# Optimization experiments

Measured on AMD Instinct MI355X. Metric: run time of the kernel, lower is better.

## Reference

```python
import jax, jax.numpy as jnp
from jax import lax
import numpy as np

ROI = 7  # roi_size


def _extract_rois(feat, coords):
    """Faithful port of extract_roi_features: clamp a 7x7 window to image bounds,
    then bilinearly resize the (possibly smaller) crop back to 7x7
    (F.interpolate, mode='bilinear', align_corners=False)."""
    B, C, H, W = feat.shape
    half = ROI // 2

    def axis_idx(c, size):
        start = jnp.maximum(0, c - half)                  # [B,A]
        end = jnp.minimum(size, c + half + 1)
        Li = end - start                                  # crop length (int) [B,A]
        L = Li.astype(feat.dtype)[..., None]              # [B,A,1]
        j = jnp.arange(ROI, dtype=feat.dtype)
        # align_corners=False source coordinate, clamped into the crop
        src = jnp.clip((j + 0.5) * L / ROI - 0.5, 0.0, L - 1.0)  # [B,A,7]
        i0 = jnp.floor(src).astype(jnp.int32)
        i1 = jnp.minimum(i0 + 1, Li[..., None] - 1)
        w1 = src - i0.astype(feat.dtype)
        return start[..., None] + i0, start[..., None] + i1, 1.0 - w1, w1

    xc = coords[..., 0].astype(jnp.int32)
    yc = coords[..., 1].astype(jnp.int32)
    y0, y1, wy0, wy1 = axis_idx(yc, H)
    x0, x1, wx0, wx1 = axis_idx(xc, W)
    Bn, A = xc.shape
    bi = jnp.arange(Bn)[:, None, None, None]

    def g(Y, X):  # gather -> [B,A,7,7,C]
        return feat[bi, :, Y[:, :, :, None], X[:, :, None, :]]

    wy0 = wy0[:, :, :, None, None]; wy1 = wy1[:, :, :, None, None]
    wx0 = wx0[:, :, None, :, None]; wx1 = wx1[:, :, None, :, None]
    v = (wy0 * wx0 * g(y0, x0) + wy0 * wx1 * g(y0, x1)
         + wy1 * wx0 * g(y1, x0) + wy1 * wx1 * g(y1, x1))
    return jnp.transpose(v, (0, 1, 4, 2, 3))  # [B,A,C,7,7]


def _conv(x, w, b, pad):
    y = lax.conv_general_dilated(x, w, (1, 1), [(pad, pad), (pad, pad)],
                                 dimension_numbers=('NCHW', 'OIHW', 'NCHW'))
    return y + b[None, :, None, None]


def _bn(x, scale, bias, mean, var, eps=1e-5):
    inv = scale * lax.rsqrt(var + eps)
    return x * inv[None, :, None, None] + (bias - mean * inv)[None, :, None, None]


def setup_inputs() -> dict:
    key = jax.random.key(0)
    ks = jax.random.split(key, 12)
    B, A, C, H, W = 8, 128, 256, 64, 64
    f32 = jnp.float32
    d = {}
    d['feat_rgb'] = jax.random.normal(ks[0], (B, C, H, W), f32)
    d['feat_tir'] = jax.random.normal(ks[1], (B, C, H, W), f32)
    d['anchor_coords'] = jax.random.randint(ks[2], (B, A, 2), 0, 64).astype(jnp.int32)
    # local_fusion: Conv(2C->C,3) BN ReLU Conv(C->C,3) BN ReLU
    d['conv1_w'] = jax.random.normal(ks[3], (C, 2 * C, 3, 3), f32) * 0.02
    d['conv1_b'] = jnp.zeros((C,), f32)
    d['bn1_scale'] = jnp.ones((C,), f32)
    d['bn1_bias'] = jnp.zeros((C,), f32)
    d['bn1_mean'] = jax.random.normal(ks[4], (C,), f32) * 0.1
    d['bn1_var'] = jax.random.uniform(ks[5], (C,), f32, 0.5, 1.5)
    d['conv2_w'] = jax.random.normal(ks[6], (C, C, 3, 3), f32) * 0.02
    d['conv2_b'] = jnp.zeros((C,), f32)
    d['bn2_scale'] = jnp.ones((C,), f32)
    d['bn2_bias'] = jnp.zeros((C,), f32)
    d['bn2_mean'] = jax.random.normal(ks[7], (C,), f32) * 0.1
    d['bn2_var'] = jax.random.uniform(ks[8], (C,), f32, 0.5, 1.5)
    # weight_generator: Conv(C->C//4,1) ReLU Conv(C//4->2,1) Softmax(dim=1)
    d['wg1_w'] = jax.random.normal(ks[9], (C // 4, C, 1, 1), f32) * 0.05
    d['wg1_b'] = jnp.zeros((C // 4,), f32)
    d['wg2_w'] = jax.random.normal(ks[10], (2, C // 4, 1, 1), f32) * 0.05
    d['wg2_b'] = jnp.zeros((2,), f32)
    return d


def reference(feat_rgb, feat_tir, anchor_coords,
              conv1_w, conv1_b, bn1_scale, bn1_bias, bn1_mean, bn1_var,
              conv2_w, conv2_b, bn2_scale, bn2_bias, bn2_mean, bn2_var,
              wg1_w, wg1_b, wg2_w, wg2_b):
    B, C, H, W = feat_rgb.shape
    A = anchor_coords.shape[1]
    roi_rgb = _extract_rois(feat_rgb, anchor_coords)  # [B,A,C,7,7]
    roi_tir = _extract_rois(feat_tir, anchor_coords)
    rgb = roi_rgb.reshape(B * A, C, ROI, ROI)
    tir = roi_tir.reshape(B * A, C, ROI, ROI)
    x = jnp.concatenate([rgb, tir], axis=1)           # [B*A, 2C, 7, 7]
    x = jax.nn.relu(_bn(_conv(x, conv1_w, conv1_b, 1), bn1_scale, bn1_bias, bn1_mean, bn1_var))
    x = jax.nn.relu(_bn(_conv(x, conv2_w, conv2_b, 1), bn2_scale, bn2_bias, bn2_mean, bn2_var))
    h = jax.nn.relu(_conv(x, wg1_w, wg1_b, 0))
    w = jax.nn.softmax(_conv(h, wg2_w, wg2_b, 0), axis=1)  # [B*A, 2, 7, 7]
    fused = w[:, 0:1] * rgb + w[:, 1:2] * tir
    return fused.reshape(B, A, C, ROI, ROI)
```

## Files before the change

kernel.cpp:

```cpp
#include <hip/hip_runtime.h>
#include <cstddef>
#include <cstdint>


typedef unsigned int u32;
typedef unsigned short u16;
typedef __attribute__((ext_vector_type(8))) short short8;
typedef __attribute__((ext_vector_type(16))) float float16v;

__device__ __forceinline__ float bf2f(u16 u) {
  u32 x = ((u32)u) << 16;
  return __builtin_bit_cast(float, x);
}
__device__ __forceinline__ u16 f2bf(float f) {
  u32 x = __builtin_bit_cast(u32, f);
  x = x + 0x7fffu + ((x >> 16) & 1u);
  return (u16)(x >> 16);
}
__device__ __forceinline__ void gl_lds16(const void* g, void* l) {
  __builtin_amdgcn_global_load_lds((const __attribute__((address_space(1))) void*)g,
                                   (__attribute__((address_space(3))) void*)l, 16, 0, 0);
}

template <int IC>
__global__ void k_prep_w(const float* __restrict__ w, u16* __restrict__ wt) {
  int i = blockIdx.x * 256 + threadIdx.x;
  if (i >= 9 * 256 * IC) return;
  int e = i & 7;
  int r = i >> 3;
  int oc = r & 255;
  int r2 = r >> 8;
  int oct = r2 % (IC / 8);
  int t = r2 / (IC / 8);
  int ic = oct * 8 + e;
  wt[i] = f2bf(w[((size_t)oc * IC + ic) * 9 + t]);
}

__global__ void k_prep_bn(const float* __restrict__ cb, const float* __restrict__ sc,
                          const float* __restrict__ bi, const float* __restrict__ mn,
                          const float* __restrict__ vr, float* __restrict__ sb) {
  int c = threadIdx.x;
  float inv = sc[c] * rsqrtf(vr[c] + 1e-5f);
  sb[c]       = inv;
  sb[256 + c] = cb[c] * inv + (bi[c] - mn[c] * inv);
}

__global__ __launch_bounds__(256)
void k_roi2(const float* __restrict__ frgb, const float* __restrict__ ftir,
            const int* __restrict__ coords, u16* __restrict__ cat) {
  int ba = blockIdx.x, b = ba >> 7, tid = threadIdx.x;
  __shared__ int   si0[2][7], si1[2][7];
  __shared__ float sw0[2][7], sw1[2][7];
  __shared__ u16 tile[49][514];
  if (tid < 14) {
    int axis = tid / 7;
    int j = tid - axis * 7;
    int c = coords[ba * 2 + (axis == 0 ? 1 : 0)];
    int start = max(0, c - 3);
    int end   = min(64, c + 4);
    int Li = end - start;
    float L = (float)Li;
    float src = ((float)j + 0.5f) * L / 7.0f - 0.5f;
    src = fminf(fmaxf(src, 0.0f), L - 1.0f);
    int i0 = (int)floorf(src);
    int i1 = min(i0 + 1, Li - 1);
    float w1 = src - (float)i0;
    si0[axis][j] = start + i0;
    si1[axis][j] = start + i1;
    sw0[axis][j] = 1.0f - w1;
    sw1[axis][j] = w1;
  }
  __syncthreads();
  const float* fr = frgb + (size_t)b * 256 * 4096;
  const float* ft = ftir + (size_t)b * 256 * 4096;
  for (int idx = tid; idx < 256 * 49; idx += 256) {
    int c = idx / 49, p = idx - c * 49;
    int jy = p / 7, jx = p - (p / 7) * 7;
    int y0 = si0[0][jy], y1 = si1[0][jy];
    int x0 = si0[1][jx], x1 = si1[1][jx];
    float wy0 = sw0[0][jy], wy1 = sw1[0][jy];
    float wx0 = sw0[1][jx], wx1 = sw1[1][jx];
    float a00 = wy0 * wx0, a01 = wy0 * wx1, a10 = wy1 * wx0, a11 = wy1 * wx1;
    const float* fc = fr + (size_t)c * 4096;
    float vr_ = a00 * fc[y0 * 64 + x0] + a01 * fc[y0 * 64 + x1] +
                a10 * fc[y1 * 64 + x0] + a11 * fc[y1 * 64 + x1];
    const float* gc = ft + (size_t)c * 4096;
    float vt_ = a00 * gc[y0 * 64 + x0] + a01 * gc[y0 * 64 + x1] +
                a10 * gc[y1 * 64 + x0] + a11 * gc[y1 * 64 + x1];
    tile[p][c]       = f2bf(vr_);
    tile[p][256 + c] = f2bf(vt_);
  }
  __syncthreads();
  u16* dst = cat + (size_t)ba * 81 * 512;
  for (int o = tid; o < 81 * 512; o += 256) {
    int row = o >> 9, c = o & 511;
    int py0 = row / 9, px0 = row - (row / 9) * 9;
    u16 v = 0;
    if (py0 >= 1 && py0 <= 7 && px0 >= 1 && px0 <= 7)
      v = tile[(py0 - 1) * 7 + (px0 - 1)][c];
    dst[o] = v;
  }
}

template <int ICT, bool FIRST>
__global__ __launch_bounds__(512, 4)
void k_conv_mfma(const u16* __restrict__ IN, const u16* __restrict__ WT,
                 const float* __restrict__ sb, u16* __restrict__ OUT) {
  constexpr int NC = ICT / 64;
  constexpr int BUFB = 2 * 81 * 128;
  __shared__ __align__(16) u16 lds[2][BUFB / 2];
  const int tid = threadIdx.x;
  const int lane = tid & 63, wv = tid >> 6;
  const int ng = wv & 3, mg = wv >> 2;
  const int l31 = lane & 31, h32 = lane >> 5;
  const int ba2 = blockIdx.x * 2;
  const char* inb = (const char*)IN;

  if (FIRST) {
    int oc = tid & 255, rh = tid >> 8;
    u16* ob = OUT + ((size_t)(ba2 + rh) * 81) * 256 + oc;
#pragma unroll
    for (int i = 0; i < 32; ++i) {
      int row = (i < 9) ? i : (i < 18) ? (63 + i)
                                       : (9 * ((i - 18) / 2 + 1) + ((i - 18) & 1) * 8);
      ob[row * 256] = 0;
    }
  }

  int rg[2];
#pragma unroll
  for (int i = 0; i < 2; ++i) {
    int P = (mg * 2 + i) * 32 + l31;
    if (P > 97) P = 97;
    int roi = (P >= 49) ? 1 : 0;
    int q = P - roi * 49;
    rg[i] = roi * 81 + (q / 7) * 9 + (q - (q / 7) * 7);
  }

  float16v acc[2][2];
#pragma unroll
  for (int i = 0; i < 2; ++i)
#pragma unroll
    for (int f = 0; f < 2; ++f)
#pragma unroll
      for (int e = 0; e < 16; ++e) acc[i][f][e] = 0.0f;

  auto stage = [&](int ch, int buf) {
    for (int s = wv; s < 21; s += 8) {
      int d = s * 1024 + lane * 16;
      if (d < BUFB) {
        int u = d ^ (((d >> 7) & 7) << 4);
        int row_g = u >> 7;
        int col = u & 127;
        int roi = (row_g >= 81) ? 1 : 0;
        int rr = row_g - roi * 81;
        const char* src = inb + ((size_t)(ba2 + roi) * 81 + rr) * (ICT * 2) +
                          ch * 128 + col;
        gl_lds16(src, (char*)&lds[buf][0] + s * 1024);
      }
    }
  };

  stage(0, 0);
  __syncthreads();

  const u16* wthr = WT + (size_t)h32 * 2048 + (size_t)(ng * 64 + l31) * 8;

  int cur = 0;
#pragma unroll 1
  for (int ch = 0; ch < NC; ++ch) {
    if (ch + 1 < NC) stage(ch + 1, cur ^ 1);
    const char* lb = (const char*)&lds[cur][0];
    const u16* wch = wthr + (size_t)ch * 8 * 2048;
#pragma unroll
    for (int t = 0; t < 9; ++t) {
      const int dy = t / 3, dx = t - (t / 3) * 3;
      short8 wfr[4][2];
#pragma unroll
      for (int kk = 0; kk < 4; ++kk)
#pragma unroll
        for (int f = 0; f < 2; ++f)
          wfr[kk][f] = *(const short8*)(wch + (size_t)(t * (ICT / 8) + kk * 2) * 2048 +
                                        f * 256);
#pragma unroll
      for (int kk = 0; kk < 4; ++kk) {
        short8 bfr[2];
#pragma unroll
        for (int i = 0; i < 2; ++i) {
          int rr = rg[i] + dy * 9 + dx;
          int byt = (rr * 128 + kk * 32 + h32 * 16) ^ ((rr & 7) << 4);
          bfr[i] = *(const short8*)(lb + byt);
        }
        __builtin_amdgcn_s_setprio(1);
#pragma unroll
        for (int i = 0; i < 2; ++i)
#pragma unroll
          for (int f = 0; f < 2; ++f)
            acc[i][f] = FIRST
                ? __builtin_amdgcn_mfma_f32_32x32x16_bf16(bfr[i], wfr[kk][f],
                                                          acc[i][f], 0, 0, 0)
                : __builtin_amdgcn_mfma_f32_32x32x16_bf16(wfr[kk][f], bfr[i],
                                                          acc[i][f], 0, 0, 0);
        __builtin_amdgcn_s_setprio(0);
      }
    }
    __syncthreads();
    cur ^= 1;
  }

  if (FIRST) {
    u16* ob = OUT + (size_t)ba2 * 81 * 256;
#pragma unroll
    for (int f = 0; f < 2; ++f) {
      int oc = ng * 64 + f * 32 + l31;
      float s = sb[oc], bb = sb[256 + oc];
#pragma unroll
      for (int i = 0; i < 2; ++i) {
        int tl = mg * 2 + i;
#pragma unroll
        for (int reg = 0; reg < 16; ++reg) {
          int m = (reg & 3) + 8 * (reg >> 2) + 4 * h32;
          int P = tl * 32 + m;
          if (P < 98) {
            int roi = (P >= 49) ? 1 : 0;
            int q = P - roi * 49;
            int pp = (q / 7 + 1) * 9 + (q - (q / 7) * 7) + 1;
            ob[((size_t)roi * 81 + pp) * 256 + oc] =
                f2bf(fmaxf(acc[i][f][reg] * s + bb, 0.0f));
          }
        }
      }
    }
  } else {
    u16* ob = OUT + (size_t)ba2 * 256 * 49;
#pragma unroll
    for (int i = 0; i < 2; ++i) {
      int tl = mg * 2 + i;
      int P = tl * 32 + l31;
      if (P < 98) {
        int roi = (P >= 49) ? 1 : 0;
        int q = P - roi * 49;
#pragma unroll
        for (int f = 0; f < 2; ++f)
#pragma unroll
          for (int reg = 0; reg < 16; ++reg) {
            int oc = ng * 64 + f * 32 + (reg & 3) + 8 * (reg >> 2) + 4 * h32;
            float s = sb[oc], bb = sb[256 + oc];
            ob[((size_t)roi * 256 + oc) * 49 + q] =
                f2bf(fmaxf(acc[i][f][reg] * s + bb, 0.0f));
          }
      }
    }
  }
}

__global__ __launch_bounds__(256)
void k_head_fuse(const u16* __restrict__ x3, const u16* __restrict__ cat,
                 const float* __restrict__ w1, const float* __restrict__ b1,
                 const float* __restrict__ w2, const float* __restrict__ b2,
                 float* __restrict__ out) {
  int ba  = blockIdx.x;
  int tid = threadIdx.x;
  __shared__ float xs[256 * 49];
  __shared__ float hs[64 * 49];
  __shared__ float ls[2 * 49];
  __shared__ float swx[2 * 49];
  const u16* src = x3 + (size_t)ba * 256 * 49;
  for (int idx = tid; idx < 256 * 49; idx += 256) xs[idx] = bf2f(src[idx]);
  __syncthreads();
  for (int idx = tid; idx < 64 * 49; idx += 256) {
    int oh = idx / 49, p = idx - oh * 49;
    float s = b1[oh];
    const float* wr = w1 + oh * 256;
    for (int ic = 0; ic < 256; ++ic) s += wr[ic] * xs[ic * 49 + p];
    hs[idx] = fmaxf(s, 0.0f);
  }
  __syncthreads();
  if (tid < 98) {
    int chn = tid / 49, p = tid - chn * 49;
    float s = b2[chn];
    const float* wr = w2 + chn * 64;
    for (int k = 0; k < 64; ++k) s += wr[k] * hs[k * 49 + p];
    ls[tid] = s;
  }
  __syncthreads();
  if (tid < 49) {
    float l0 = ls[tid], l1 = ls[49 + tid];
    float m = fmaxf(l0, l1);
    float e0 = expf(l0 - m), e1 = expf(l1 - m);
    float d = e0 + e1;
    swx[tid]      = e0 / d;
    swx[49 + tid] = e1 / d;
  }
  __syncthreads();
  const u16* cr = cat + (size_t)ba * 81 * 512;
  float* o = out + (size_t)ba * 256 * 49;
  for (int idx = tid; idx < 256 * 49; idx += 256) {
    int c = idx / 49, p = idx - (idx / 49) * 49;
    int pp = (p / 7 + 1) * 9 + (p - (p / 7) * 7) + 1;
    float rgb = bf2f(cr[pp * 512 + c]);
    float tir = bf2f(cr[pp * 512 + 256 + c]);
    o[idx] = swx[p] * rgb + swx[49 + p] * tir;
  }
}

extern "C" void kernel_launch(void* const* d_in, const int* in_sizes, int n_in,
                              void* d_out, int out_size, void* d_ws, size_t ws_size,
                              hipStream_t stream) {
  const float* feat_rgb = (const float*)d_in[0];
  const float* feat_tir = (const float*)d_in[1];
  const int*   coords   = (const int*)d_in[2];
  const float* conv1_w  = (const float*)d_in[3];
  const float* conv1_b  = (const float*)d_in[4];
  const float* bn1_s    = (const float*)d_in[5];
  const float* bn1_b    = (const float*)d_in[6];
  const float* bn1_m    = (const float*)d_in[7];
  const float* bn1_v    = (const float*)d_in[8];
  const float* conv2_w  = (const float*)d_in[9];
  const float* conv2_b  = (const float*)d_in[10];
  const float* bn2_s    = (const float*)d_in[11];
  const float* bn2_b    = (const float*)d_in[12];
  const float* bn2_m    = (const float*)d_in[13];
  const float* bn2_v    = (const float*)d_in[14];
  const float* wg1_w    = (const float*)d_in[15];
  const float* wg1_b    = (const float*)d_in[16];
  const float* wg2_w    = (const float*)d_in[17];
  const float* wg2_b    = (const float*)d_in[18];
  float* out = (float*)d_out;

  char* base = (char*)d_ws;
  u16*   W1T  = (u16*)(base);
  u16*   W2T  = (u16*)(base + 2359296);
  float* SB1  = (float*)(base + 2359296 + 1179648);
  float* SB2  = (float*)(base + 2359296 + 1179648 + 2048);
  u16*   CAT2 = (u16*)(base + 2359296 + 1179648 + 4096);
  u16*   X2   = (u16*)(base + 2359296 + 1179648 + 4096 + 84934656);
  u16*   X3   = (u16*)(base + 2359296 + 1179648 + 4096 + 84934656 + 42467328);

  k_prep_w<512><<<(9 * 256 * 512 + 255) / 256, 256, 0, stream>>>(conv1_w, W1T);
  k_prep_w<256><<<(9 * 256 * 256 + 255) / 256, 256, 0, stream>>>(conv2_w, W2T);
  k_prep_bn<<<1, 256, 0, stream>>>(conv1_b, bn1_s, bn1_b, bn1_m, bn1_v, SB1);
  k_prep_bn<<<1, 256, 0, stream>>>(conv2_b, bn2_s, bn2_b, bn2_m, bn2_v, SB2);
  k_roi2<<<1024, 256, 0, stream>>>(feat_rgb, feat_tir, coords, CAT2);
  k_conv_mfma<512, true><<<512, 512, 0, stream>>>(CAT2, W1T, SB1, X2);
  k_conv_mfma<256, false><<<512, 512, 0, stream>>>(X2, W2T, SB2, X3);
  k_head_fuse<<<1024, 256, 0, stream>>>(X3, CAT2, wg1_w, wg1_b, wg2_w, wg2_b, out);
}
```

Baseline: 616.9 us.

## Store activations unpadded and apply conv zero-padding in LDS

Measured after the change: 640.2 us. +3.8%, slower.

```diff
diff --git a/kernel.cpp b/kernel.cpp
--- a/kernel.cpp
+++ b/kernel.cpp
@@ -91,14 +91,10 @@
     tile[p][256 + c] = f2bf(vt_);
   }
   __syncthreads();
-  u16* dst = cat + (size_t)ba * 81 * 512;
-  for (int o = tid; o < 81 * 512; o += 256) {
+  u16* dst = cat + (size_t)ba * 49 * 512;
+  for (int o = tid; o < 49 * 512; o += 256) {
     int row = o >> 9, c = o & 511;
-    int py0 = row / 9, px0 = row - (row / 9) * 9;
-    u16 v = 0;
-    if (py0 >= 1 && py0 <= 7 && px0 >= 1 && px0 <= 7)
-      v = tile[(py0 - 1) * 7 + (px0 - 1)][c];
-    dst[o] = v;
+    dst[o] = tile[row][c];
   }
 }
 
@@ -107,7 +103,8 @@
 void k_conv_mfma(const u16* __restrict__ IN, const u16* __restrict__ WT,
                  const float* __restrict__ sb, u16* __restrict__ OUT) {
   constexpr int NC = ICT / 64;
-  constexpr int BUFB = 2 * 81 * 128;
+  constexpr int ROIB = 137 * 128;
+  constexpr int BUFB = 2 * ROIB;
   __shared__ __align__(16) u16 lds[2][BUFB / 2];
   const int tid = threadIdx.x;
   const int lane = tid & 63, wv = tid >> 6;
@@ -116,16 +113,12 @@
   const int ba2 = blockIdx.x * 2;
   const char* inb = (const char*)IN;
 
-  if (FIRST) {
-    int oc = tid & 255, rh = tid >> 8;
-    u16* ob = OUT + ((size_t)(ba2 + rh) * 81) * 256 + oc;
-#pragma unroll
-    for (int i = 0; i < 32; ++i) {
-      int row = (i < 9) ? i : (i < 18) ? (63 + i)
-                                       : (9 * ((i - 18) / 2 + 1) + ((i - 18) & 1) * 8);
-      ob[row * 256] = 0;
-    }
-  }
+  {
+    short8 zz = (short8){0, 0, 0, 0, 0, 0, 0, 0};
+    short8* lp = (short8*)&lds[0][0];
+    for (int z = tid; z < (2 * BUFB) / 16; z += 512) lp[z] = zz;
+  }
+  __syncthreads();
 
   int rg[2];
 #pragma unroll
@@ -134,7 +127,8 @@
     if (P > 97) P = 97;
     int roi = (P >= 49) ? 1 : 0;
     int q = P - roi * 49;
-    rg[i] = roi * 81 + (q / 7) * 9 + (q - (q / 7) * 7);
+    int qy = q / 7, qx = q - (q / 7) * 7;
+    rg[i] = roi * 137 + qy * 16 + qx;
   }
 
   float16v acc[2][2];
@@ -146,17 +140,16 @@
       for (int e = 0; e < 16; ++e) acc[i][f][e] = 0.0f;
 
   auto stage = [&](int ch, int buf) {
-    for (int s = wv; s < 21; s += 8) {
-      int d = s * 1024 + lane * 16;
-      if (d < BUFB) {
-        int u = d ^ (((d >> 7) & 7) << 4);
-        int row_g = u >> 7;
-        int col = u & 127;
-        int roi = (row_g >= 81) ? 1 : 0;
-        int rr = row_g - roi * 81;
-        const char* src = inb + ((size_t)(ba2 + roi) * 81 + rr) * (ICT * 2) +
-                          ch * 128 + col;
-        gl_lds16(src, (char*)&lds[buf][0] + s * 1024);
+    for (int s = wv; s < 14; s += 8) {
+      int roi = s / 7, qy = s - roi * 7;
+      char* dbase = (char*)&lds[buf][0] + roi * ROIB + ((qy + 1) * 16 + 1) * 128;
+      if (lane < 56) {
+        int r = roi * 137 + (qy + 1) * 16 + 1 + (lane >> 3);
+        int cl = ((lane & 7) * 16) ^ ((r & 7) << 4);
+        const char* src = inb +
+            ((size_t)((ba2 + roi) * 49 + qy * 7 + (lane >> 3))) * (ICT * 2) +
+            ch * 128 + cl;
+        gl_lds16(src, dbase);
       }
     }
   };
@@ -172,44 +165,50 @@
     if (ch + 1 < NC) stage(ch + 1, cur ^ 1);
     const char* lb = (const char*)&lds[cur][0];
     const u16* wch = wthr + (size_t)ch * 8 * 2048;
-#pragma unroll
-    for (int t = 0; t < 9; ++t) {
-      const int dy = t / 3, dx = t - (t / 3) * 3;
-      short8 wfr[4][2];
-#pragma unroll
-      for (int kk = 0; kk < 4; ++kk)
+
+    short8 wfr[4][2];
+#pragma unroll
+    for (int jp = 0; jp < 3; ++jp)
+#pragma unroll
+      for (int f = 0; f < 2; ++f)
+        wfr[jp][f] = *(const short8*)(
+            wch + (size_t)(jp * 2) * 2048 + f * 256);
+#pragma unroll
+    for (int j = 0; j < 36; ++j) {
+      if (j + 3 < 36) {
+        const int jn = j + 3;
 #pragma unroll
         for (int f = 0; f < 2; ++f)
-          wfr[kk][f] = *(const short8*)(wch + (size_t)(t * (ICT / 8) + kk * 2) * 2048 +
-                                        f * 256);
-#pragma unroll
-      for (int kk = 0; kk < 4; ++kk) {
-        short8 bfr[2];
-#pragma unroll
-        for (int i = 0; i < 2; ++i) {
-          int rr = rg[i] + dy * 9 + dx;
-          int byt = (rr * 128 + kk * 32 + h32 * 16) ^ ((rr & 7) << 4);
-          bfr[i] = *(const short8*)(lb + byt);
-        }
-        __builtin_amdgcn_s_setprio(1);
-#pragma unroll
-        for (int i = 0; i < 2; ++i)
-#pragma unroll
-          for (int f = 0; f < 2; ++f)
-            acc[i][f] = FIRST
-                ? __builtin_amdgcn_mfma_f32_32x32x16_bf16(bfr[i], wfr[kk][f],
-                                                          acc[i][f], 0, 0, 0)
-                : __builtin_amdgcn_mfma_f32_32x32x16_bf16(wfr[kk][f], bfr[i],
-                                                          acc[i][f], 0, 0, 0);
-        __builtin_amdgcn_s_setprio(0);
-      }
+          wfr[jn & 3][f] = *(const short8*)(
+              wch + (size_t)((jn >> 2) * (ICT / 8) + (jn & 3) * 2) * 2048 + f * 256);
+      }
+      const int t = j >> 2, kk = j & 3;
+      const int toff = (t / 3) * 16 + (t - (t / 3) * 3);
+      short8 bfr[2];
+#pragma unroll
+      for (int i = 0; i < 2; ++i) {
+        int r = rg[i] + toff;
+        int byt = r * 128 + ((kk * 32 + h32 * 16) ^ ((r & 7) << 4));
+        bfr[i] = *(const short8*)(lb + byt);
+      }
+      __builtin_amdgcn_s_setprio(1);
+#pragma unroll
+      for (int i = 0; i < 2; ++i)
+#pragma unroll
+        for (int f = 0; f < 2; ++f)
+          acc[i][f] = FIRST
+              ? __builtin_amdgcn_mfma_f32_32x32x16_bf16(bfr[i], wfr[j & 3][f],
+                                                        acc[i][f], 0, 0, 0)
+              : __builtin_amdgcn_mfma_f32_32x32x16_bf16(wfr[j & 3][f], bfr[i],
+                                                        acc[i][f], 0, 0, 0);
+      __builtin_amdgcn_s_setprio(0);
     }
     __syncthreads();
     cur ^= 1;
   }
 
   if (FIRST) {
-    u16* ob = OUT + (size_t)ba2 * 81 * 256;
+    u16* ob = OUT + (size_t)ba2 * 49 * 256;
 #pragma unroll
     for (int f = 0; f < 2; ++f) {
       int oc = ng * 64 + f * 32 + l31;
@@ -224,8 +223,7 @@
           if (P < 98) {
             int roi = (P >= 49) ? 1 : 0;
             int q = P - roi * 49;
-            int pp = (q / 7 + 1) * 9 + (q - (q / 7) * 7) + 1;
-            ob[((size_t)roi * 81 + pp) * 256 + oc] =
+            ob[((size_t)roi * 49 + q) * 256 + oc] =
                 f2bf(fmaxf(acc[i][f][reg] * s + bb, 0.0f));
           }
         }
@@ -293,13 +291,12 @@
     swx[49 + tid] = e1 / d;
   }
   __syncthreads();
-  const u16* cr = cat + (size_t)ba * 81 * 512;
+  const u16* cr = cat + (size_t)ba * 49 * 512;
   float* o = out + (size_t)ba * 256 * 49;
   for (int idx = tid; idx < 256 * 49; idx += 256) {
     int c = idx / 49, p = idx - (idx / 49) * 49;
-    int pp = (p / 7 + 1) * 9 + (p - (p / 7) * 7) + 1;
-    float rgb = bf2f(cr[pp * 512 + c]);
-    float tir = bf2f(cr[pp * 512 + 256 + c]);
+    float rgb = bf2f(cr[p * 512 + c]);
+    float tir = bf2f(cr[p * 512 + 256 + c]);
     o[idx] = swx[p] * rgb + swx[49 + p] * tir;
   }
 }
@@ -333,16 +330,16 @@
   u16*   W2T  = (u16*)(base + 2359296);
   float* SB1  = (float*)(base + 2359296 + 1179648);
   float* SB2  = (float*)(base + 2359296 + 1179648 + 2048);
-  u16*   CAT2 = (u16*)(base + 2359296 + 1179648 + 4096);
-  u16*   X2   = (u16*)(base + 2359296 + 1179648 + 4096 + 84934656);
-  u16*   X3   = (u16*)(base + 2359296 + 1179648 + 4096 + 84934656 + 42467328);
+  u16*   CAT  = (u16*)(base + 3543040);
+  u16*   X2   = (u16*)(base + 3543040 + 51380224);
+  u16*   X3   = (u16*)(base + 3543040 + 51380224 + 25690112);
 
   k_prep_w<512><<<(9 * 256 * 512 + 255) / 256, 256, 0, stream>>>(conv1_w, W1T);
   k_prep_w<256><<<(9 * 256 * 256 + 255) / 256, 256, 0, stream>>>(conv2_w, W2T);
   k_prep_bn<<<1, 256, 0, stream>>>(conv1_b, bn1_s, bn1_b, bn1_m, bn1_v, SB1);
   k_prep_bn<<<1, 256, 0, stream>>>(conv2_b, bn2_s, bn2_b, bn2_m, bn2_v, SB2);
-  k_roi2<<<1024, 256, 0, stream>>>(feat_rgb, feat_tir, coords, CAT2);
-  k_conv_mfma<512, true><<<512, 512, 0, stream>>>(CAT2, W1T, SB1, X2);
+  k_roi2<<<1024, 256, 0, stream>>>(feat_rgb, feat_tir, coords, CAT);
+  k_conv_mfma<512, true><<<512, 512, 0, stream>>>(CAT, W1T, SB1, X2);
   k_conv_mfma<256, false><<<512, 512, 0, stream>>>(X2, W2T, SB2, X3);
-  k_head_fuse<<<1024, 256, 0, stream>>>(X3, CAT2, wg1_w, wg1_b, wg2_w, wg2_b, out);
-}
+  k_head_fuse<<<1024, 256, 0, stream>>>(X3, CAT, wg1_w, wg1_b, wg2_w, wg2_b, out);
+}
```
